# Kernel optimization log

Hardware: AMD Instinct MI355X
Metric: run time of the kernel (lower is better)

The kernel has to match this reference:

```python
import jax, jax.numpy as jnp
import numpy as np

NUM_HEADS = 12
N_TOKENS = 1

def setup_inputs() -> dict:
    key = jax.random.key(0)
    ks = jax.random.split(key, 13)
    D = 768
    s = 0.02
    return {
        "x": jax.random.normal(ks[0], (64, 1025, D), jnp.float32),
        "qW": jax.random.normal(ks[1], (D, D), jnp.float32) * s,
        "qb": jax.random.normal(ks[2], (D,), jnp.float32) * s,
        "kW": jax.random.normal(ks[3], (D, D), jnp.float32) * s,
        "kb": jax.random.normal(ks[4], (D,), jnp.float32) * s,
        "vW": jax.random.normal(ks[5], (D, D), jnp.float32) * s,
        "vb": jax.random.normal(ks[6], (D,), jnp.float32) * s,
        "w1W": jax.random.normal(ks[7], (NUM_HEADS, NUM_HEADS), jnp.float32) * 0.1,
        "w1b": jax.random.normal(ks[8], (NUM_HEADS,), jnp.float32) * 0.1,
        "w2W": jax.random.normal(ks[9], (NUM_HEADS, NUM_HEADS), jnp.float32) * 0.1,
        "w2b": jax.random.normal(ks[10], (NUM_HEADS,), jnp.float32) * 0.1,
        "projW": jax.random.normal(ks[11], (D, D), jnp.float32) * s,
        "projb": jax.random.normal(ks[12], (D,), jnp.float32) * s,
    }

def reference(x, qW, qb, kW, kb, vW, vb, w1W, w1b, w2W, w2b, projW, projb):
    B, N, C = x.shape  # C == embed_dim == 768
    H = NUM_HEADS
    d = C // H
    scale = d ** -0.5
    cls = x[:, :N_TOKENS]  # [B, n, C]
    # torch Linear: y = x @ W.T + b
    q = (cls @ qW.T + qb).reshape(B, N_TOKENS, H, d).transpose(0, 2, 1, 3) * scale  # [B,H,n,d]
    k = (x @ kW.T + kb).reshape(B, N, H, d).transpose(0, 2, 1, 3)  # [B,H,N,d]
    v = (x @ vW.T + vb).reshape(B, N, H, d).transpose(0, 2, 1, 3)  # [B,H,N,d]
    attn = jnp.einsum('bhqd,bhkd->bhqk', q, k)  # [B,H,n,N]
    # talking-heads pre-softmax: linear over head dim, added residually
    attn = attn + jnp.einsum('bhqk,gh->bgqk', attn, w1W) + w1b[None, :, None, None]
    attn = jax.nn.softmax(attn, axis=-1)
    # talking-heads post-softmax
    attn = attn + jnp.einsum('bhqk,gh->bgqk', attn, w2W) + w2b[None, :, None, None]
    out = jnp.einsum('bhqk,bhkd->bhqd', attn, v)  # [B,H,n,d]
    out = out.transpose(0, 2, 1, 3).reshape(B, N_TOKENS, C)
    return out @ projW.T + projb
```

## Files before the change

### kernel.cpp

```cpp
#include <hip/hip_runtime.h>
#include <hip/hip_bf16.h>

#define B 64
#define N 1025
#define C 768
#define H 12
#define HD 64
#define TILES 17

__device__ __forceinline__ float wave_reduce_add(float v) {
    #pragma unroll
    for (int m = 1; m < 64; m <<= 1) v += __shfl_xor(v, m, 64);
    return v;
}

__global__ __launch_bounds__(256) void k_qproj(const float* __restrict__ x,
                                               const float* __restrict__ qW,
                                               const float* __restrict__ qb,
                                               float* __restrict__ qout) {
    __shared__ float cls[4 * C];
    int bt = blockIdx.x, ct = blockIdx.y, tid = threadIdx.x;
    for (int i = tid; i < 768; i += 256) {
        int bl = i / 192, c4 = i % 192;
        ((float4*)cls)[i] = ((const float4*)(x + (size_t)(bt * 4 + bl) * N * C))[c4];
    }
    __syncthreads();
    int w = tid >> 6, lane = tid & 63;
    int b = bt * 4 + w;
    const float* clsrow = &cls[w * C];
    for (int cl = 0; cl < 16; ++cl) {
        int c = ct * 16 + cl;
        const float4* wr = (const float4*)(qW + (size_t)c * C + lane * 12);
        const float4* xr = (const float4*)(clsrow + lane * 12);
        float acc = 0.f;
        #pragma unroll
        for (int s = 0; s < 3; ++s) {
            float4 a = wr[s], v = xr[s];
            acc += a.x * v.x + a.y * v.y + a.z * v.z + a.w * v.w;
        }
        acc = wave_reduce_add(acc);
        if (lane == 0) qout[b * C + c] = 0.125f * (acc + qb[c]);
    }
}

__global__ __launch_bounds__(256) void k_qk(const float* __restrict__ q,
                                            const float* __restrict__ kW,
                                            const float* __restrict__ kb,
                                            float* __restrict__ qk,
                                            float* __restrict__ qkb) {
    int bt = blockIdx.x, h = blockIdx.y, tid = threadIdx.x;
    if (tid < 192) {
        float4 acc[4] = {};
        #pragma unroll 4
        for (int i = 0; i < HD; ++i) {
            int row = h * HD + i;
            float4 kv = *(const float4*)(kW + (size_t)row * C + tid * 4);
            #pragma unroll
            for (int bl = 0; bl < 4; ++bl) {
                float qv = q[(bt * 4 + bl) * C + row];
                acc[bl].x += qv * kv.x; acc[bl].y += qv * kv.y;
                acc[bl].z += qv * kv.z; acc[bl].w += qv * kv.w;
            }
        }
        #pragma unroll
        for (int bl = 0; bl < 4; ++bl) {
            int b = bt * 4 + bl;
            *(float4*)(qk + ((size_t)b * H + h) * C + tid * 4) = acc[bl];
        }
    }
    int w = tid >> 6, lane = tid & 63;
    int b = bt * 4 + w;
    float v = q[b * C + h * HD + lane] * kb[h * HD + lane];
    v = wave_reduce_add(v);
    if (lane == 0) qkb[b * H + h] = v;
}

__global__ __launch_bounds__(256) void k_att(const float* __restrict__ x,
                                             const float* __restrict__ qk,
                                             const float* __restrict__ qkbias,
                                             const float* __restrict__ w1W,
                                             const float* __restrict__ w1b,
                                             __hip_bfloat16* __restrict__ ype,
                                             float* __restrict__ ypx,
                                             float* __restrict__ sstat) {
    __shared__ float qs[12 * C];
    __shared__ float w1s[144], w1bs[12], qbs[12];
    int tile = blockIdx.x, b = blockIdx.y, tid = threadIdx.x;
    const float4* qksrc = (const float4*)(qk + (size_t)b * H * C);
    for (int i = tid; i < 2304; i += 256) ((float4*)qs)[i] = qksrc[i];
    if (tid < 144) w1s[tid] = w1W[tid];
    if (tid < 12)  { w1bs[tid] = w1b[tid]; qbs[tid] = qkbias[b * 12 + tid]; }

    int lane = tid & 63, w = tid >> 6;
    int c16 = lane & 15, r = lane >> 4;
    int rowbase = tile * 64 + w * 16 + r * 4;
    const float* xb = x + (size_t)b * N * C;
    const float4 z4 = make_float4(0.f, 0.f, 0.f, 0.f);

    float4 xcur[4], xnxt[4];
    #pragma unroll
    for (int j = 0; j < 4; ++j) {
        int row = rowbase + j;
        xcur[j] = (row < N) ? *(const float4*)(xb + (size_t)row * C + c16 * 4) : z4;
    }
    __syncthreads();

    float acc[4][12] = {};
    for (int cc = 0; cc < 12; ++cc) {
        if (cc < 11) {
            int cn = (cc + 1) * 64 + c16 * 4;
            #pragma unroll
            for (int j = 0; j < 4; ++j) {
                int row = rowbase + j;
                xnxt[j] = (row < N) ? *(const float4*)(xb + (size_t)row * C + cn) : z4;
            }
        }
        int cq = cc * 64 + c16 * 4;
        #pragma unroll
        for (int h = 0; h < 12; ++h) {
            float4 q0 = *(const float4*)(qs + h * C + cq);
            #pragma unroll
            for (int j = 0; j < 4; ++j)
                acc[j][h] += xcur[j].x * q0.x + xcur[j].y * q0.y +
                             xcur[j].z * q0.z + xcur[j].w * q0.w;
        }
        if (cc < 11) {
            #pragma unroll
            for (int j = 0; j < 4; ++j) xcur[j] = xnxt[j];
        }
    }
    #pragma unroll
    for (int j = 0; j < 4; ++j)
        #pragma unroll
        for (int h = 0; h < 12; ++h) {
            float v = acc[j][h];
            v += __shfl_xor(v, 1); v += __shfl_xor(v, 2);
            v += __shfl_xor(v, 4); v += __shfl_xor(v, 8);
            acc[j][h] = v;
        }
    __syncthreads();
    if (c16 == 0) {
        #pragma unroll
        for (int j = 0; j < 4; ++j)
            #pragma unroll
            for (int h = 0; h < 12; ++h)
                qs[(w * 16 + r * 4 + j) * 12 + h] = acc[j][h];
    }
    __syncthreads();
    if (tid < 64) {
        int row = tile * 64 + tid;
        bool valid = row < N;
        float s_[12], e[12];
        #pragma unroll
        for (int h = 0; h < 12; ++h) s_[h] = qs[tid * 12 + h] + qbs[h];
        #pragma unroll
        for (int g = 0; g < 12; ++g) {
            float a = s_[g] + w1bs[g];
            #pragma unroll
            for (int h = 0; h < 12; ++h) a += w1s[g * 12 + h] * s_[h];
            e[g] = valid ? __expf(a) : 0.f;
        }
        #pragma unroll
        for (int g = 0; g < 12; ++g) qs[tid * 12 + g] = e[g];
        #pragma unroll
        for (int g = 0; g < 12; ++g) {
            float sg = wave_reduce_add(e[g]);
            if (tid == 0) sstat[((size_t)b * TILES + tile) * 12 + g] = sg;
        }
    }
    __syncthreads();

    float pacc[12][3] = {};
    float xs[3] = {0.f, 0.f, 0.f};
    int nv = N - tile * 64; if (nv > 64) nv = 64;
    for (int n0 = 0; n0 < 64; n0 += 4) {
        float xv[4][3];
        #pragma unroll
        for (int u = 0; u < 4; ++u) {
            int n = n0 + u;
            const float* xr = xb + (size_t)(tile * 64 + n) * C + tid;
            bool val = n < nv;
            xv[u][0] = val ? xr[0]   : 0.f;
            xv[u][1] = val ? xr[256] : 0.f;
            xv[u][2] = val ? xr[512] : 0.f;
        }
        #pragma unroll
        for (int u = 0; u < 4; ++u) {
            const float* er = qs + (n0 + u) * 12;
            xs[0] += xv[u][0]; xs[1] += xv[u][1]; xs[2] += xv[u][2];
            #pragma unroll
            for (int h = 0; h < 12; ++h) {
                float ev = er[h];
                pacc[h][0] += ev * xv[u][0];
                pacc[h][1] += ev * xv[u][1];
                pacc[h][2] += ev * xv[u][2];
            }
        }
    }
    size_t base = (size_t)tile * B + b;
    #pragma unroll
    for (int h = 0; h < 12; ++h) {
        __hip_bfloat16* dst = ype + (base * 12 + h) * C + tid;
        dst[0]   = __float2bfloat16(pacc[h][0]);
        dst[256] = __float2bfloat16(pacc[h][1]);
        dst[512] = __float2bfloat16(pacc[h][2]);
    }
    float* xdst = ypx + base * C + tid;
    xdst[0] = xs[0]; xdst[256] = xs[1]; xdst[512] = xs[2];
}

__global__ __launch_bounds__(256) void k_combine(const __hip_bfloat16* __restrict__ ype,
                                                 const float* __restrict__ ypx,
                                                 const float* __restrict__ sstat,
                                                 const float* __restrict__ w2W,
                                                 const float* __restrict__ w2b,
                                                 float* __restrict__ ybar) {
    __shared__ float w2s[144], w2bs[12], ish[12];
    int cg = blockIdx.x, b = blockIdx.y, tid = threadIdx.x;
    if (tid < 144) w2s[tid] = w2W[tid];
    if (tid < 12) {
        w2bs[tid] = w2b[tid];
        float S = 0.f;
        #pragma unroll
        for (int t = 0; t < TILES; ++t) S += sstat[((size_t)b * TILES + t) * 12 + tid];
        ish[tid] = 1.f / S;
    }
    __syncthreads();
    int c = cg * 256 + tid;
    float P[12] = {};
    float X = 0.f;
    for (int t = 0; t < TILES; ++t) {
        size_t base = (size_t)t * B + b;
        const __hip_bfloat16* src = ype + base * 12 * C + c;
        #pragma unroll
        for (int h = 0; h < 12; ++h) P[h] += __bfloat162float(src[h * C]);
        X += ypx[base * C + c];
    }
    #pragma unroll
    for (int h = 0; h < 12; ++h) P[h] *= ish[h];
    #pragma unroll
    for (int g = 0; g < 12; ++g) {
        float a = P[g] + w2bs[g] * X;
        #pragma unroll
        for (int h = 0; h < 12; ++h) a += w2s[g * 12 + h] * P[h];
        ybar[((size_t)b * 12 + g) * C + c] = a;
    }
}

__global__ __launch_bounds__(256) void k_zproj(const float* __restrict__ ybar,
                                               const float* __restrict__ vW,
                                               const float* __restrict__ vb,
                                               const float* __restrict__ w2W,
                                               const float* __restrict__ w2b,
                                               float* __restrict__ z) {
    __shared__ float ys[4 * C];
    int bt = blockIdx.x, h = blockIdx.y, tid = threadIdx.x;
    for (int i = tid; i < 768; i += 256) {
        int bl = i / 192, c4 = i % 192;
        int b = bt * 4 + bl;
        ((float4*)ys)[i] = ((const float4*)(ybar + ((size_t)b * 12 + h) * C))[c4];
    }
    __syncthreads();
    float sv = 1.f + 1025.f * w2b[h];
    #pragma unroll
    for (int j = 0; j < 12; ++j) sv += w2W[h * 12 + j];
    int w = tid >> 6, lane = tid & 63;
    int b = bt * 4 + w;
    const float* yrow = &ys[w * C];
    for (int cl = 0; cl < 64; ++cl) {
        int c = h * 64 + cl;
        const float4* wr = (const float4*)(vW + (size_t)c * C + lane * 12);
        const float4* yr = (const float4*)(yrow + lane * 12);
        float acc = 0.f;
        #pragma unroll
        for (int s = 0; s < 3; ++s) {
            float4 a = wr[s], v = yr[s];
            acc += a.x * v.x + a.y * v.y + a.z * v.z + a.w * v.w;
        }
        acc = wave_reduce_add(acc);
        if (lane == 0) z[b * C + c] = acc + vb[c] * sv;
    }
}

__global__ __launch_bounds__(256) void k_out(const float* __restrict__ z,
                                             const float* __restrict__ pW,
                                             const float* __restrict__ pb,
                                             float* __restrict__ out) {
    __shared__ float zs[4 * C];
    int bt = blockIdx.x, ct = blockIdx.y, tid = threadIdx.x;
    for (int i = tid; i < 768; i += 256)
        ((float4*)zs)[i] = ((const float4*)(z + (size_t)bt * 4 * C))[i];
    __syncthreads();
    int w = tid >> 6, lane = tid & 63;
    int b = bt * 4 + w;
    for (int cl = 0; cl < 16; ++cl) {
        int c = ct * 16 + cl;
        const float4* wr = (const float4*)(pW + (size_t)c * C + lane * 12);
        const float4* zr = (const float4*)(zs + w * C + lane * 12);
        float acc = 0.f;
        #pragma unroll
        for (int s = 0; s < 3; ++s) {
            float4 a = wr[s], v = zr[s];
            acc += a.x * v.x + a.y * v.y + a.z * v.z + a.w * v.w;
        }
        acc = wave_reduce_add(acc);
        if (lane == 0) out[b * C + c] = acc + pb[c];
    }
}

extern "C" void kernel_launch(void* const* d_in, const int* in_sizes, int n_in,
                              void* d_out, int out_size, void* d_ws, size_t ws_size,
                              hipStream_t stream) {
    const float* x    = (const float*)d_in[0];
    const float* qW   = (const float*)d_in[1];
    const float* qb   = (const float*)d_in[2];
    const float* kW   = (const float*)d_in[3];
    const float* kb   = (const float*)d_in[4];
    const float* vW   = (const float*)d_in[5];
    const float* vb   = (const float*)d_in[6];
    const float* w1W  = (const float*)d_in[7];
    const float* w1b  = (const float*)d_in[8];
    const float* w2W  = (const float*)d_in[9];
    const float* w2b  = (const float*)d_in[10];
    const float* pW   = (const float*)d_in[11];
    const float* pb   = (const float*)d_in[12];
    float* out = (float*)d_out;

    float* ws    = (float*)d_ws;
    float* qk    = ws + 0;
    float* qkb   = ws + 589824;
    float* q     = ws + 590592;
    float* sstat = ws + 639744;
    float* ypx   = ws + 652800;
    __hip_bfloat16* ype = (__hip_bfloat16*)(ws + 1488384);
    float* ybar  = qk;
    float* z     = q;

    k_qproj  <<<dim3(16, 48), 256, 0, stream>>>(x, qW, qb, q);
    k_qk     <<<dim3(16, 12), 256, 0, stream>>>(q, kW, kb, qk, qkb);
    k_att    <<<dim3(17, 64), 256, 0, stream>>>(x, qk, qkb, w1W, w1b, ype, ypx, sstat);
    k_combine<<<dim3(3, 64),  256, 0, stream>>>(ype, ypx, sstat, w2W, w2b, ybar);
    k_zproj  <<<dim3(16, 12), 256, 0, stream>>>(ybar, vW, vb, w2W, w2b, z);
    k_out    <<<dim3(16, 48), 256, 0, stream>>>(z, pW, pb, out);
}
```

Before: 498.5 us.

## Widen attention blocks to 512 threads and split combine/zproj work across more blocks

The attention kernel now runs 512 threads per block. Each thread handles 2 rows instead of 4 in the score pass, using a three-buffer x prefetch, and half the heads in the weighted-sum pass. The combine kernel splits the 17 tiles across four thread groups and reduces their partials through shared memory, giving 12 column groups instead of 3. The z projection splits each head's 64 output columns over four blocks. The aim is more parallelism and occupancy in the memory-bound stages, at the cost of redundant x reads per half and extra shared-memory reductions.

```diff
diff --git a/kernel.cpp b/kernel.cpp
--- a/kernel.cpp
+++ b/kernel.cpp
@@ -75,62 +75,64 @@
     if (lane == 0) qkb[b * H + h] = v;
 }
 
-__global__ __launch_bounds__(256) void k_att(const float* __restrict__ x,
-                                             const float* __restrict__ qk,
-                                             const float* __restrict__ qkbias,
-                                             const float* __restrict__ w1W,
-                                             const float* __restrict__ w1b,
-                                             __hip_bfloat16* __restrict__ ype,
-                                             float* __restrict__ ypx,
-                                             float* __restrict__ sstat) {
+#define LOADX(buf, ccol)                                                       \
+    {                                                                          \
+        _Pragma("unroll")                                                      \
+        for (int j = 0; j < 2; ++j) {                                          \
+            int row_ = rowbase + j;                                            \
+            buf[j] = (row_ < N) ? *(const float4*)(xb + (size_t)row_ * C +     \
+                                                   (ccol) + c16 * 4)           \
+                                : z4;                                          \
+        }                                                                      \
+    }
+#define FMAS(buf, cq)                                                          \
+    {                                                                          \
+        _Pragma("unroll")                                                      \
+        for (int h = 0; h < 12; ++h) {                                         \
+            float4 q0 = *(const float4*)(qs + h * C + (cq) + c16 * 4);         \
+            _Pragma("unroll")                                                  \
+            for (int j = 0; j < 2; ++j)                                        \
+                acc[j][h] += buf[j].x * q0.x + buf[j].y * q0.y +               \
+                             buf[j].z * q0.z + buf[j].w * q0.w;                \
+        }                                                                      \
+    }
+
+__global__ __launch_bounds__(512, 6) void k_att(const float* __restrict__ x,
+                                                const float* __restrict__ qk,
+                                                const float* __restrict__ qkbias,
+                                                const float* __restrict__ w1W,
+                                                const float* __restrict__ w1b,
+                                                __hip_bfloat16* __restrict__ ype,
+                                                float* __restrict__ ypx,
+                                                float* __restrict__ sstat) {
     __shared__ float qs[12 * C];
     __shared__ float w1s[144], w1bs[12], qbs[12];
     int tile = blockIdx.x, b = blockIdx.y, tid = threadIdx.x;
     const float4* qksrc = (const float4*)(qk + (size_t)b * H * C);
-    for (int i = tid; i < 2304; i += 256) ((float4*)qs)[i] = qksrc[i];
+    for (int i = tid; i < 2304; i += 512) ((float4*)qs)[i] = qksrc[i];
     if (tid < 144) w1s[tid] = w1W[tid];
     if (tid < 12)  { w1bs[tid] = w1b[tid]; qbs[tid] = qkbias[b * 12 + tid]; }
 
     int lane = tid & 63, w = tid >> 6;
     int c16 = lane & 15, r = lane >> 4;
-    int rowbase = tile * 64 + w * 16 + r * 4;
+    int rowbase = tile * 64 + w * 8 + r * 2;
     const float* xb = x + (size_t)b * N * C;
     const float4 z4 = make_float4(0.f, 0.f, 0.f, 0.f);
 
-    float4 xcur[4], xnxt[4];
-    #pragma unroll
-    for (int j = 0; j < 4; ++j) {
-        int row = rowbase + j;
-        xcur[j] = (row < N) ? *(const float4*)(xb + (size_t)row * C + c16 * 4) : z4;
-    }
-    __syncthreads();
-
-    float acc[4][12] = {};
-    for (int cc = 0; cc < 12; ++cc) {
-        if (cc < 11) {
-            int cn = (cc + 1) * 64 + c16 * 4;
-            #pragma unroll
-            for (int j = 0; j < 4; ++j) {
-                int row = rowbase + j;
-                xnxt[j] = (row < N) ? *(const float4*)(xb + (size_t)row * C + cn) : z4;
-            }
-        }
-        int cq = cc * 64 + c16 * 4;
-        #pragma unroll
-        for (int h = 0; h < 12; ++h) {
-            float4 q0 = *(const float4*)(qs + h * C + cq);
-            #pragma unroll
-            for (int j = 0; j < 4; ++j)
-                acc[j][h] += xcur[j].x * q0.x + xcur[j].y * q0.y +
-                             xcur[j].z * q0.z + xcur[j].w * q0.w;
-        }
-        if (cc < 11) {
-            #pragma unroll
-            for (int j = 0; j < 4; ++j) xcur[j] = xnxt[j];
-        }
-    }
-    #pragma unroll
-    for (int j = 0; j < 4; ++j)
+    float4 xA[2], xB[2], xC[2];
+    LOADX(xA, 0); LOADX(xB, 64); LOADX(xC, 128);
+    __syncthreads();
+
+    float acc[2][12] = {};
+    #pragma unroll
+    for (int g = 0; g < 4; ++g) {
+        int cq = g * 192;
+        FMAS(xA, cq);       if (g < 3) LOADX(xA, cq + 192);
+        FMAS(xB, cq + 64);  if (g < 3) LOADX(xB, cq + 256);
+        FMAS(xC, cq + 128); if (g < 3) LOADX(xC, cq + 320);
+    }
+    #pragma unroll
+    for (int j = 0; j < 2; ++j)
         #pragma unroll
         for (int h = 0; h < 12; ++h) {
             float v = acc[j][h];
@@ -141,10 +143,10 @@
     __syncthreads();
     if (c16 == 0) {
         #pragma unroll
-        for (int j = 0; j < 4; ++j)
+        for (int j = 0; j < 2; ++j)
             #pragma unroll
             for (int h = 0; h < 12; ++h)
-                qs[(w * 16 + r * 4 + j) * 12 + h] = acc[j][h];
+                qs[(w * 8 + r * 2 + j) * 12 + h] = acc[j][h];
     }
     __syncthreads();
     if (tid < 64) {
@@ -170,7 +172,9 @@
     }
     __syncthreads();
 
-    float pacc[12][3] = {};
+    int half = tid >> 8, t = tid & 255;
+    int hb = half * 6;
+    float pacc[6][3] = {};
     float xs[3] = {0.f, 0.f, 0.f};
     int nv = N - tile * 64; if (nv > 64) nv = 64;
     for (int n0 = 0; n0 < 64; n0 += 4) {
@@ -178,7 +182,7 @@
         #pragma unroll
         for (int u = 0; u < 4; ++u) {
             int n = n0 + u;
-            const float* xr = xb + (size_t)(tile * 64 + n) * C + tid;
+            const float* xr = xb + (size_t)(tile * 64 + n) * C + t;
             bool val = n < nv;
             xv[u][0] = val ? xr[0]   : 0.f;
             xv[u][1] = val ? xr[256] : 0.f;
@@ -186,27 +190,29 @@
         }
         #pragma unroll
         for (int u = 0; u < 4; ++u) {
-            const float* er = qs + (n0 + u) * 12;
+            const float* er = qs + (n0 + u) * 12 + hb;
             xs[0] += xv[u][0]; xs[1] += xv[u][1]; xs[2] += xv[u][2];
             #pragma unroll
-            for (int h = 0; h < 12; ++h) {
-                float ev = er[h];
-                pacc[h][0] += ev * xv[u][0];
-                pacc[h][1] += ev * xv[u][1];
-                pacc[h][2] += ev * xv[u][2];
+            for (int hh = 0; hh < 6; ++hh) {
+                float ev = er[hh];
+                pacc[hh][0] += ev * xv[u][0];
+                pacc[hh][1] += ev * xv[u][1];
+                pacc[hh][2] += ev * xv[u][2];
             }
         }
     }
     size_t base = (size_t)tile * B + b;
     #pragma unroll
-    for (int h = 0; h < 12; ++h) {
-        __hip_bfloat16* dst = ype + (base * 12 + h) * C + tid;
-        dst[0]   = __float2bfloat16(pacc[h][0]);
-        dst[256] = __float2bfloat16(pacc[h][1]);
-        dst[512] = __float2bfloat16(pacc[h][2]);
-    }
-    float* xdst = ypx + base * C + tid;
-    xdst[0] = xs[0]; xdst[256] = xs[1]; xdst[512] = xs[2];
+    for (int hh = 0; hh < 6; ++hh) {
+        __hip_bfloat16* dst = ype + (base * 12 + hb + hh) * C + t;
+        dst[0]   = __float2bfloat16(pacc[hh][0]);
+        dst[256] = __float2bfloat16(pacc[hh][1]);
+        dst[512] = __float2bfloat16(pacc[hh][2]);
+    }
+    if (half == 0) {
+        float* xdst = ypx + base * C + t;
+        xdst[0] = xs[0]; xdst[256] = xs[1]; xdst[512] = xs[2];
+    }
 }
 
 __global__ __launch_bounds__(256) void k_combine(const __hip_bfloat16* __restrict__ ype,
@@ -216,7 +222,10 @@
                                                  const float* __restrict__ w2b,
                                                  float* __restrict__ ybar) {
     __shared__ float w2s[144], w2bs[12], ish[12];
+    __shared__ float part[4][64][13];
     int cg = blockIdx.x, b = blockIdx.y, tid = threadIdx.x;
+    int tg = tid >> 6, c64 = tid & 63;
+    int c = cg * 64 + c64;
     if (tid < 144) w2s[tid] = w2W[tid];
     if (tid < 12) {
         w2bs[tid] = w2b[tid];
@@ -225,11 +234,10 @@
         for (int t = 0; t < TILES; ++t) S += sstat[((size_t)b * TILES + t) * 12 + tid];
         ish[tid] = 1.f / S;
     }
-    __syncthreads();
-    int c = cg * 256 + tid;
+    int t0 = tg * 4, tend = (tg == 3) ? TILES : tg * 4 + 4;
     float P[12] = {};
     float X = 0.f;
-    for (int t = 0; t < TILES; ++t) {
+    for (int t = t0; t < tend; ++t) {
         size_t base = (size_t)t * B + b;
         const __hip_bfloat16* src = ype + base * 12 * C + c;
         #pragma unroll
@@ -237,13 +245,23 @@
         X += ypx[base * C + c];
     }
     #pragma unroll
-    for (int h = 0; h < 12; ++h) P[h] *= ish[h];
-    #pragma unroll
-    for (int g = 0; g < 12; ++g) {
-        float a = P[g] + w2bs[g] * X;
-        #pragma unroll
-        for (int h = 0; h < 12; ++h) a += w2s[g * 12 + h] * P[h];
-        ybar[((size_t)b * 12 + g) * C + c] = a;
+    for (int h = 0; h < 12; ++h) part[tg][c64][h] = P[h];
+    part[tg][c64][12] = X;
+    __syncthreads();
+    if (tg == 0) {
+        #pragma unroll
+        for (int h = 0; h < 12; ++h)
+            P[h] = (part[0][c64][h] + part[1][c64][h] +
+                    part[2][c64][h] + part[3][c64][h]) * ish[h];
+        X = part[0][c64][12] + part[1][c64][12] +
+            part[2][c64][12] + part[3][c64][12];
+        #pragma unroll
+        for (int g = 0; g < 12; ++g) {
+            float a = P[g] + w2bs[g] * X;
+            #pragma unroll
+            for (int h = 0; h < 12; ++h) a += w2s[g * 12 + h] * P[h];
+            ybar[((size_t)b * 12 + g) * C + c] = a;
+        }
     }
 }
 
@@ -254,7 +272,8 @@
                                                const float* __restrict__ w2b,
                                                float* __restrict__ z) {
     __shared__ float ys[4 * C];
-    int bt = blockIdx.x, h = blockIdx.y, tid = threadIdx.x;
+    int bt = blockIdx.x, h = blockIdx.y >> 2, cq = blockIdx.y & 3;
+    int tid = threadIdx.x;
     for (int i = tid; i < 768; i += 256) {
         int bl = i / 192, c4 = i % 192;
         int b = bt * 4 + bl;
@@ -267,8 +286,8 @@
     int w = tid >> 6, lane = tid & 63;
     int b = bt * 4 + w;
     const float* yrow = &ys[w * C];
-    for (int cl = 0; cl < 64; ++cl) {
-        int c = h * 64 + cl;
+    for (int cl = 0; cl < 16; ++cl) {
+        int c = h * 64 + cq * 16 + cl;
         const float4* wr = (const float4*)(vW + (size_t)c * C + lane * 12);
         const float4* yr = (const float4*)(yrow + lane * 12);
         float acc = 0.f;
@@ -338,8 +357,8 @@
 
     k_qproj  <<<dim3(16, 48), 256, 0, stream>>>(x, qW, qb, q);
     k_qk     <<<dim3(16, 12), 256, 0, stream>>>(q, kW, kb, qk, qkb);
-    k_att    <<<dim3(17, 64), 256, 0, stream>>>(x, qk, qkb, w1W, w1b, ype, ypx, sstat);
-    k_combine<<<dim3(3, 64),  256, 0, stream>>>(ype, ypx, sstat, w2W, w2b, ybar);
-    k_zproj  <<<dim3(16, 12), 256, 0, stream>>>(ybar, vW, vb, w2W, w2b, z);
+    k_att    <<<dim3(17, 64), 512, 0, stream>>>(x, qk, qkb, w1W, w1b, ype, ypx, sstat);
+    k_combine<<<dim3(12, 64), 256, 0, stream>>>(ype, ypx, sstat, w2W, w2b, ybar);
+    k_zproj  <<<dim3(16, 48), 256, 0, stream>>>(ybar, vW, vb, w2W, w2b, z);
     k_out    <<<dim3(16, 48), 256, 0, stream>>>(z, pW, pb, out);
 }
```

Result: slower. 1.084 ms (+117.5%).
